# Optimization experiments

Hardware: AMD Instinct MI355X
Metric: run time of the kernel (lower is better)

The kernel has to match this reference:

```python
import jax, jax.numpy as jnp
import numpy as np

B, N, D = 8, 1024, 512
H, DH = 8, 64
CH, CD = 6, 64  # ck/cv come in as (b, 6, n, 64); 6*64 = opn_inner_dim = 384
ID = H * DH    # inner_dim = 512
SCALE = DH ** -0.5


def _l2norm_dim1(x):
    # F.normalize(x, dim=1): normalize over the token axis of (b, n, c)
    return x / jnp.maximum(jnp.linalg.norm(x, axis=1, keepdims=True), 1e-12)


def _style_vectorizer(c, ws, bs):
    b, h, n, d = c.shape
    x = c.transpose(0, 2, 1, 3).reshape(b, n, h * d)
    x = _l2norm_dim1(x)
    for w, bi in zip(ws, bs):
        x = jax.nn.leaky_relu(x @ w.T + bi, 0.2)
    return x.reshape(b, n, H, DH).transpose(0, 2, 1, 3)


def _mlp_block(x, w, b):
    # x: (b, H, n, DH) -> rearr, normalize over n, Linear+GELU(exact), rearr back
    bb, h, n, d = x.shape
    y = x.transpose(0, 2, 1, 3).reshape(bb, n, h * d)
    y = _l2norm_dim1(y)
    y = jax.nn.gelu(y @ w.T + b, approximate=False)
    return y.reshape(bb, n, H, DH).transpose(0, 2, 1, 3)


def setup_inputs() -> dict:
    key = jax.random.key(0)
    ks = jax.random.split(key, 24)
    s = 0.02  # keep attention logits well-conditioned
    return {
        "x": jax.random.normal(ks[0], (B, N, D), jnp.float32),
        "ck": jax.random.normal(ks[1], (B, CH, N, CD), jnp.float32),
        "cv": jax.random.normal(ks[2], (B, CH, N, CD), jnp.float32),
        "w_qkv": jax.random.normal(ks[3], (3 * ID, D), jnp.float32) * s,
        "w_out": jax.random.normal(ks[4], (D, ID), jnp.float32) * s,
        "b_out": jnp.zeros((D,), jnp.float32),
        "ckw0": jax.random.normal(ks[5], (ID, CH * CD), jnp.float32) * s,
        "ckb0": jnp.zeros((ID,), jnp.float32),
        "ckw1": jax.random.normal(ks[6], (ID, ID), jnp.float32) * s,
        "ckb1": jnp.zeros((ID,), jnp.float32),
        "ckw2": jax.random.normal(ks[7], (ID, ID), jnp.float32) * s,
        "ckb2": jnp.zeros((ID,), jnp.float32),
        "cvw0": jax.random.normal(ks[8], (ID, CH * CD), jnp.float32) * s,
        "cvb0": jnp.zeros((ID,), jnp.float32),
        "cvw1": jax.random.normal(ks[9], (ID, ID), jnp.float32) * s,
        "cvb1": jnp.zeros((ID,), jnp.float32),
        "cvw2": jax.random.normal(ks[10], (ID, ID), jnp.float32) * s,
        "cvb2": jnp.zeros((ID,), jnp.float32),
        "nl_w": jax.random.normal(ks[11], (ID, ID), jnp.float32) * s,
        "nl_b": jnp.zeros((ID,), jnp.float32),
        "sub_ratio": jax.random.normal(ks[12], (1, H, 1, DH), jnp.float32) + 1.0,
    }


def reference(x, ck, cv, w_qkv, w_out, b_out,
              ckw0, ckb0, ckw1, ckb1, ckw2, ckb2,
              cvw0, cvb0, cvw1, cvb1, cvw2, cvb2,
              nl_w, nl_b, sub_ratio):
    b, n, _ = x.shape
    qkv = x @ w_qkv.T                      # (b, n, 3*ID)
    q, k, v = jnp.split(qkv, 3, axis=-1)
    to_h = lambda t: t.reshape(b, n, H, DH).transpose(0, 2, 1, 3)  # (b,H,n,DH)
    q, k, v = to_h(q), to_h(k), to_h(v)

    # standard self-attention branch
    dots = jnp.einsum("bhnd,bhmd->bhnm", q, k) * SCALE
    out = jnp.einsum("bhnm,bhmd->bhnd", jax.nn.softmax(dots, axis=-1), v)

    # context (correction) branch
    ckh = _style_vectorizer(ck, (ckw0, ckw1, ckw2), (ckb0, ckb1, ckb2))
    cvh = _style_vectorizer(cv, (cvw0, cvw1, cvw2), (cvb0, cvb1, cvb2))
    dots_c = jnp.einsum("bhnd,bhmd->bhnm", q, ckh) * SCALE
    out_c = jnp.einsum("bhnm,bhmd->bhnd", jax.nn.softmax(dots_c, axis=-1), cvh)
    out_c = _mlp_block(out_c, nl_w, nl_b)

    out = out - out_c * sub_ratio          # elementwise scale-subtract combine
    out = out.transpose(0, 2, 1, 3).reshape(b, n, ID)
    return out @ w_out.T + b_out
```

## Files before the change

kernel.cpp:

```cpp
#include <hip/hip_runtime.h>
#include <hip/hip_fp16.h>
#include <math.h>

typedef _Float16 h16_t;
typedef __attribute__((ext_vector_type(4))) _Float16 h16x4;
typedef __attribute__((ext_vector_type(8))) _Float16 h16x8;
typedef __attribute__((ext_vector_type(4))) float f32x4;

static_assert(sizeof(h16_t) == 2, "f16 size");

__device__ __forceinline__ f32x4 mfma16(h16x8 a, h16x8 b, f32x4 c) {
  return __builtin_amdgcn_mfma_f32_16x16x32_f16(a, b, c, 0, 0, 0);
}

struct CvtArgs {
  const float* src[10];
  h16_t* dst[10];
  int start4[10];
  int total4;
};

__global__ __launch_bounds__(256) void k_cvt_multi(CvtArgs a) {
  const int i4 = blockIdx.x * 256 + threadIdx.x;
  if (i4 >= a.total4) return;
  int seg = 0;
#pragma unroll
  for (int t = 1; t < 10; ++t) seg += (i4 >= a.start4[t]) ? 1 : 0;
  const int off = (i4 - a.start4[seg]) * 4;
  const float4 v = *(const float4*)(a.src[seg] + off);
  h16x4 o;
  o[0] = (h16_t)v.x; o[1] = (h16_t)v.y; o[2] = (h16_t)v.z; o[3] = (h16_t)v.w;
  *(h16x4*)(a.dst[seg] + off) = o;
}

template <int K>
__device__ __forceinline__ void gemm_run(const h16_t* __restrict__ A,
                                         const h16_t* __restrict__ W,
                                         int m0, int o0, h16_t* wl, f32x4* acc) {
  constexpr int NS = K / 128;
  const int lane = threadIdx.x & 63;
  const int l15 = lane & 15;
  const int quad = lane >> 4;
  int sr[4], sc[4], sd[4];
#pragma unroll
  for (int i = 0; i < 4; ++i) {
    const int id = threadIdx.x + i * 256;
    const int row = id >> 4, c = id & 15;
    sr[i] = row;
    sc[i] = c * 8;
    sd[i] = (row * 16 + (c ^ (row & 7))) * 8;
  }
  h16x8 wr[4];
#pragma unroll
  for (int i = 0; i < 4; ++i)
    wr[i] = *(const h16x8*)(W + (size_t)(o0 + sr[i]) * K + sc[i]);
#pragma unroll
  for (int i = 0; i < 4; ++i) *(h16x8*)(wl + sd[i]) = wr[i];
  __syncthreads();
#pragma unroll
  for (int sg = 0; sg < NS; ++sg) {
    if (sg + 1 < NS) {
#pragma unroll
      for (int i = 0; i < 4; ++i)
        wr[i] = *(const h16x8*)(W + (size_t)(o0 + sr[i]) * K + (sg + 1) * 128 + sc[i]);
    }
    const h16_t* ap = A + (size_t)(m0 + l15) * K + sg * 128 + quad * 8;
    const h16_t* wp = wl + (sg & 1) * 8192;
#pragma unroll
    for (int ks = 0; ks < 4; ++ks) {
      h16x8 af = *(const h16x8*)(ap + ks * 32);
#pragma unroll
      for (int j = 0; j < 4; ++j) {
        h16x8 wf = *(const h16x8*)(
            wp + (size_t)((j * 16 + l15) * 16 + ((ks * 4 + quad) ^ (l15 & 7))) * 8);
        acc[j] = mfma16(af, wf, acc[j]);
      }
    }
    if (sg + 1 < NS) {
      h16_t* wn = wl + ((sg + 1) & 1) * 8192;
#pragma unroll
      for (int i = 0; i < 4; ++i) *(h16x8*)(wn + sd[i]) = wr[i];
    }
    __syncthreads();
  }
}

#define EPILOGUE_SETUP()                            \
  const int wv = threadIdx.x >> 6;                  \
  const int lane = threadIdx.x & 63;                \
  const int l15 = lane & 15;                        \
  const int quad = lane >> 4;                       \
  const int m0 = blockIdx.x * 64 + wv * 16;         \
  const int o0 = blockIdx.y * 64;                   \
  f32x4 acc[4];                                     \
  for (int j = 0; j < 4; ++j) acc[j] = f32x4{0.f, 0.f, 0.f, 0.f};

__global__ __launch_bounds__(256) void k_gemm_qkv(
    const h16_t* __restrict__ X, const h16_t* __restrict__ W,
    h16_t* __restrict__ qb, h16_t* __restrict__ kb, h16_t* __restrict__ vT) {
  __shared__ h16_t wl[2 * 8192];
  EPILOGUE_SETUP();
  gemm_run<512>(X, W, m0, o0, wl, acc);
#pragma unroll
  for (int j = 0; j < 4; ++j)
#pragma unroll
    for (int r = 0; r < 4; ++r) {
      const int o = o0 + j * 16 + l15;
      const int m = m0 + quad * 4 + r;
      const int b = m >> 10, n = m & 1023;
      const int oo = o & 511, h = oo >> 6, d = oo & 63;
      const size_t bh = (size_t)(b * 8 + h);
      const h16_t v = (h16_t)acc[j][r];
      if (o < 512)
        qb[(bh * 1024 + n) * 64 + d] = v;
      else if (o < 1024)
        kb[(bh * 1024 + n) * 64 + d] = v;
      else
        vT[(bh * 64 + d) * 1024 + n] = v;
    }
}

struct Leaky2Args {
  const h16_t* A0; const h16_t* W0; const float* b0; h16_t* Y0;
  const h16_t* A1; const h16_t* W1; const float* b1; h16_t* Y1;
};

template <int K, int L0, int L1>
__global__ __launch_bounds__(256) void k_gemm_leaky2(Leaky2Args g) {
  __shared__ h16_t wl[2 * 8192];
  const int zz = blockIdx.z;
  const h16_t* A = zz ? g.A1 : g.A0;
  const h16_t* W = zz ? g.W1 : g.W0;
  const float* bias = zz ? g.b1 : g.b0;
  h16_t* Y = zz ? g.Y1 : g.Y0;
  EPILOGUE_SETUP();
  gemm_run<K>(A, W, m0, o0, wl, acc);
  const int LAYOUT = zz ? L1 : L0;
#pragma unroll
  for (int j = 0; j < 4; ++j)
#pragma unroll
    for (int r = 0; r < 4; ++r) {
      const int o = o0 + j * 16 + l15;
      const int m = m0 + quad * 4 + r;
      float v = acc[j][r] + bias[o];
      v = v > 0.f ? v : 0.2f * v;
      if (LAYOUT == 0) {
        Y[(size_t)m * 512 + o] = (h16_t)v;
      } else {
        const int b = m >> 10, n = m & 1023;
        const int h = o >> 6, d = o & 63;
        if (LAYOUT == 1)
          Y[((size_t)(b * 8 + h) * 1024 + n) * 64 + d] = (h16_t)v;
        else
          Y[((size_t)(b * 8 + h) * 64 + d) * 1024 + n] = (h16_t)v;
      }
    }
}

__global__ __launch_bounds__(256) void k_gemm_nl(
    const h16_t* __restrict__ A, const h16_t* __restrict__ W,
    const float* __restrict__ bias, const h16_t* __restrict__ attn,
    const float* __restrict__ subr, h16_t* __restrict__ Y) {
  __shared__ h16_t wl[2 * 8192];
  EPILOGUE_SETUP();
  gemm_run<512>(A, W, m0, o0, wl, acc);
#pragma unroll
  for (int j = 0; j < 4; ++j)
#pragma unroll
    for (int r = 0; r < 4; ++r) {
      const int o = o0 + j * 16 + l15;
      const int m = m0 + quad * 4 + r;
      const float v = acc[j][r] + bias[o];
      const float g = 0.5f * v * (1.f + erff(v * 0.70710678118654752f));
      const float res = (float)attn[(size_t)m * 512 + o] - g * subr[o];
      Y[(size_t)m * 512 + o] = (h16_t)res;
    }
}

__global__ __launch_bounds__(256) void k_gemm_out(
    const h16_t* __restrict__ A, const h16_t* __restrict__ W,
    const float* __restrict__ bias, float* __restrict__ Y) {
  __shared__ h16_t wl[2 * 8192];
  EPILOGUE_SETUP();
  gemm_run<512>(A, W, m0, o0, wl, acc);
#pragma unroll
  for (int j = 0; j < 4; ++j)
#pragma unroll
    for (int r = 0; r < 4; ++r) {
      const int o = o0 + j * 16 + l15;
      const int m = m0 + quad * 4 + r;
      Y[(size_t)m * 512 + o] = acc[j][r] + bias[o];
    }
}

__global__ __launch_bounds__(256) void k_attn4(
    const h16_t* __restrict__ q,
    const h16_t* __restrict__ k0, const h16_t* __restrict__ v0, h16_t* __restrict__ out0,
    const h16_t* __restrict__ k1, const h16_t* __restrict__ v1, h16_t* __restrict__ out1) {
  const int wv = threadIdx.x >> 6;
  const int lane = threadIdx.x & 63;
  const int l15 = lane & 15;
  const int quad = lane >> 4;
  const int bh = blockIdx.y, b = bh >> 3, h = bh & 7;
  const h16_t* kb = (blockIdx.z ? k1 : k0) + (size_t)bh * 65536;
  const h16_t* vb = (blockIdx.z ? v1 : v0) + (size_t)bh * 65536;
  h16_t* out = blockIdx.z ? out1 : out0;

  __shared__ h16_t kls[2 * 4096];
  __shared__ h16_t vls[2 * 4096];

  const int q0r = blockIdx.x * 128 + wv * 32;
  h16x8 qa[2][2];
#pragma unroll
  for (int t = 0; t < 2; ++t)
#pragma unroll
    for (int s = 0; s < 2; ++s)
      qa[t][s] = *(const h16x8*)(q + ((size_t)bh * 1024 + q0r + t * 16 + l15) * 64 + s * 32 + quad * 8);

  int ksrc[2], vsrc[2], ldst[2];
#pragma unroll
  for (int i = 0; i < 2; ++i) {
    const int L = threadIdx.x + i * 256;
    const int row = L >> 3, cs = L & 7;
    const int key = ((row & 3) << 1) | ((row >> 3) & 1);
    const int c = cs ^ key;
    ksrc[i] = row * 64 + c * 8;
    vsrc[i] = row * 1024 + c * 8;
    ldst[i] = L * 8;
  }

  int kfo[2][4], vfo[2][4];
#pragma unroll
  for (int s = 0; s < 2; ++s)
#pragma unroll
    for (int nt = 0; nt < 4; ++nt) {
      const int r = (nt & 1) * 32 + (l15 >> 2) * 8 + (nt >> 1) * 4 + (l15 & 3);
      const int kk = ((r & 3) << 1) | ((r >> 3) & 1);
      kfo[s][nt] = (r * 8 + ((s * 4 + quad) ^ kk)) * 8;
      const int d = nt * 16 + l15;
      const int kd = ((d & 3) << 1) | ((d >> 3) & 1);
      vfo[s][nt] = (d * 8 + ((s * 4 + quad) ^ kd)) * 8;
    }

  f32x4 oaT[2][4];
#pragma unroll
  for (int t = 0; t < 2; ++t)
#pragma unroll
    for (int j = 0; j < 4; ++j) oaT[t][j] = f32x4{0.f, 0.f, 0.f, 0.f};
  float l_part[2] = {0.f, 0.f};

  h16x8 kr[2], vr[2];
#pragma unroll
  for (int i = 0; i < 2; ++i) {
    kr[i] = *(const h16x8*)(kb + ksrc[i]);
    vr[i] = *(const h16x8*)(vb + vsrc[i]);
  }
#pragma unroll
  for (int i = 0; i < 2; ++i) {
    *(h16x8*)(kls + ldst[i]) = kr[i];
    *(h16x8*)(vls + ldst[i]) = vr[i];
  }
  __syncthreads();

  for (int mt = 0; mt < 16; ++mt) {
    const int cur = (mt & 1) * 4096;
    if (mt < 15) {
      const int mm1 = (mt + 1) * 64;
#pragma unroll
      for (int i = 0; i < 2; ++i) {
        kr[i] = *(const h16x8*)(kb + mm1 * 64 + ksrc[i]);
        vr[i] = *(const h16x8*)(vb + mm1 + vsrc[i]);
      }
    }

    f32x4 sfT[2][4];
#pragma unroll
    for (int t = 0; t < 2; ++t)
#pragma unroll
      for (int j = 0; j < 4; ++j) sfT[t][j] = f32x4{0.f, 0.f, 0.f, 0.f};
#pragma unroll
    for (int s = 0; s < 2; ++s)
#pragma unroll
      for (int nt = 0; nt < 4; ++nt) {
        h16x8 kf = *(const h16x8*)(kls + cur + kfo[s][nt]);
        sfT[0][nt] = mfma16(kf, qa[0][s], sfT[0][nt]);
        sfT[1][nt] = mfma16(kf, qa[1][s], sfT[1][nt]);
      }
    int pk[2][4][2];
#pragma unroll
    for (int t = 0; t < 2; ++t)
#pragma unroll
      for (int nt = 0; nt < 4; ++nt) {
        const float e0 = __expf(sfT[t][nt][0] * 0.125f);
        const float e1 = __expf(sfT[t][nt][1] * 0.125f);
        const float e2 = __expf(sfT[t][nt][2] * 0.125f);
        const float e3 = __expf(sfT[t][nt][3] * 0.125f);
        l_part[t] += (e0 + e1) + (e2 + e3);
        pk[t][nt][0] = __builtin_bit_cast(int, __builtin_amdgcn_cvt_pkrtz(e0, e1));
        pk[t][nt][1] = __builtin_bit_cast(int, __builtin_amdgcn_cvt_pkrtz(e2, e3));
      }
#pragma unroll
    for (int s = 0; s < 2; ++s) {
      int4 b0 = {pk[0][s][0], pk[0][s][1], pk[0][s + 2][0], pk[0][s + 2][1]};
      int4 b1 = {pk[1][s][0], pk[1][s][1], pk[1][s + 2][0], pk[1][s + 2][1]};
      h16x8 bf0 = __builtin_bit_cast(h16x8, b0);
      h16x8 bf1 = __builtin_bit_cast(h16x8, b1);
#pragma unroll
      for (int nt = 0; nt < 4; ++nt) {
        h16x8 vf = *(const h16x8*)(vls + cur + vfo[s][nt]);
        oaT[0][nt] = mfma16(vf, bf0, oaT[0][nt]);
        oaT[1][nt] = mfma16(vf, bf1, oaT[1][nt]);
      }
    }

    if (mt < 15) {
      const int nxt = ((mt + 1) & 1) * 4096;
#pragma unroll
      for (int i = 0; i < 2; ++i) {
        *(h16x8*)(kls + nxt + ldst[i]) = kr[i];
        *(h16x8*)(vls + nxt + ldst[i]) = vr[i];
      }
    }
    __syncthreads();
  }
#pragma unroll
  for (int t = 0; t < 2; ++t) {
    float l = l_part[t] + __shfl_xor(l_part[t], 16, 64);
    l += __shfl_xor(l, 32, 64);
    const float iv = 1.f / l;
    h16_t* obase = out + ((size_t)b * 1024 + q0r + t * 16 + l15) * 512 + h * 64 + quad * 4;
#pragma unroll
    for (int nt = 0; nt < 4; ++nt) {
      h16x4 o;
#pragma unroll
      for (int r = 0; r < 4; ++r) o[r] = (h16_t)(oaT[t][nt][r] * iv);
      *(h16x4*)(obase + nt * 16) = o;
    }
  }
}

__global__ __launch_bounds__(384) void k_cn_ck_p1(const float* __restrict__ c0,
                                                  const float* __restrict__ c1,
                                                  float* __restrict__ part) {
  const int b = blockIdx.x, ch = blockIdx.y, z = blockIdx.z, f = threadIdx.x;
  const float* c = z ? c1 : c0;
  const int h = f >> 6, d = f & 63;
  const float* p = c + ((size_t)(b * 6 + h) * 1024 + ch * 16) * 64 + d;
  float s = 0.f;
#pragma unroll
  for (int n = 0; n < 16; ++n) {
    const float v = p[(size_t)n * 64];
    s += v * v;
  }
  part[(size_t)z * 196608 + (size_t)(b * 64 + ch) * 384 + f] = s;
}

__global__ __launch_bounds__(384) void k_cn_ck_p2(const float* __restrict__ part,
                                                  float* __restrict__ inv) {
  const int b = blockIdx.x, z = blockIdx.y, f = threadIdx.x;
  float s = 0.f;
#pragma unroll 8
  for (int ch = 0; ch < 64; ++ch)
    s += part[(size_t)z * 196608 + (size_t)(b * 64 + ch) * 384 + f];
  inv[z * 3072 + b * 384 + f] = 1.f / fmaxf(sqrtf(s), 1e-12f);
}

__global__ __launch_bounds__(384) void k_norm_ck(const float* __restrict__ c0,
                                                 const float* __restrict__ c1,
                                                 const float* __restrict__ inv,
                                                 h16_t* __restrict__ y0,
                                                 h16_t* __restrict__ y1) {
  const int bn = blockIdx.x, z = blockIdx.y, f = threadIdx.x;
  const float* c = z ? c1 : c0;
  h16_t* out = z ? y1 : y0;
  const int b = bn >> 10, n = bn & 1023;
  const int h = f >> 6, d = f & 63;
  out[(size_t)bn * 384 + f] =
      (h16_t)(c[((size_t)(b * 6 + h) * 1024 + n) * 64 + d] * inv[z * 3072 + b * 384 + f]);
}

__global__ __launch_bounds__(512) void k_cn_rm_p1(const h16_t* __restrict__ a,
                                                  float* __restrict__ part) {
  const int b = blockIdx.x, ch = blockIdx.y, f = threadIdx.x;
  const h16_t* p = a + ((size_t)b * 1024 + ch * 16) * 512 + f;
  float s = 0.f;
#pragma unroll
  for (int n = 0; n < 16; ++n) {
    const float v = (float)p[(size_t)n * 512];
    s += v * v;
  }
  part[(size_t)(b * 64 + ch) * 512 + f] = s;
}

__global__ __launch_bounds__(512) void k_cn_rm_p2(const float* __restrict__ part,
                                                  float* __restrict__ inv) {
  const int b = blockIdx.x, f = threadIdx.x;
  float s = 0.f;
#pragma unroll 8
  for (int ch = 0; ch < 64; ++ch) s += part[(size_t)(b * 64 + ch) * 512 + f];
  inv[b * 512 + f] = 1.f / fmaxf(sqrtf(s), 1e-12f);
}

__global__ __launch_bounds__(512) void k_norm_rm(const h16_t* __restrict__ a,
                                                 const float* __restrict__ inv,
                                                 h16_t* __restrict__ out) {
  const int bn = blockIdx.x, f = threadIdx.x;
  const int b = bn >> 10;
  out[(size_t)bn * 512 + f] = (h16_t)((float)a[(size_t)bn * 512 + f] * inv[b * 512 + f]);
}

extern "C" void kernel_launch(void* const* d_in, const int* in_sizes, int n_in,
                              void* d_out, int out_size, void* d_ws, size_t ws_size,
                              hipStream_t stream) {
  (void)in_sizes; (void)n_in; (void)out_size; (void)ws_size;
  const float* x     = (const float*)d_in[0];
  const float* ck    = (const float*)d_in[1];
  const float* cv    = (const float*)d_in[2];
  const float* w_qkv = (const float*)d_in[3];
  const float* w_out = (const float*)d_in[4];
  const float* b_out = (const float*)d_in[5];
  const float* ckw0  = (const float*)d_in[6];
  const float* ckb0  = (const float*)d_in[7];
  const float* ckw1  = (const float*)d_in[8];
  const float* ckb1  = (const float*)d_in[9];
  const float* ckw2  = (const float*)d_in[10];
  const float* ckb2  = (const float*)d_in[11];
  const float* cvw0  = (const float*)d_in[12];
  const float* cvb0  = (const float*)d_in[13];
  const float* cvw1  = (const float*)d_in[14];
  const float* cvb1  = (const float*)d_in[15];
  const float* cvw2  = (const float*)d_in[16];
  const float* cvb2  = (const float*)d_in[17];
  const float* nl_w  = (const float*)d_in[18];
  const float* nl_b  = (const float*)d_in[19];
  const float* subr  = (const float*)d_in[20];

  const size_t MB = 1024 * 1024;
  char* p = (char*)d_ws;
  float* inv1 = (float*)p;
  float* part = (float*)(p + 64 * 1024);
  h16_t* S0 = (h16_t*)(p + 2 * MB + 0 * 8 * MB);
  h16_t* S1 = (h16_t*)(p + 2 * MB + 1 * 8 * MB);
  h16_t* S2 = (h16_t*)(p + 2 * MB + 2 * 8 * MB);
  h16_t* S3 = (h16_t*)(p + 2 * MB + 3 * 8 * MB);
  h16_t* S4 = (h16_t*)(p + 2 * MB + 4 * 8 * MB);
  h16_t* S5 = (h16_t*)(p + 2 * MB + 5 * 8 * MB);
  h16_t* WBASE = (h16_t*)(p + 50 * MB);
  h16_t* w_qkvb = WBASE;
  h16_t* w_outb = w_qkvb + 786432;
  h16_t* ckw0b  = w_outb + 262144;
  h16_t* ckw1b  = ckw0b + 196608;
  h16_t* ckw2b  = ckw1b + 262144;
  h16_t* cvw0b  = ckw2b + 262144;
  h16_t* cvw1b  = cvw0b + 196608;
  h16_t* cvw2b  = cvw1b + 262144;
  h16_t* nl_wb  = cvw2b + 262144;
  h16_t* T0   = (h16_t*)d_out;
  h16_t* T1   = (h16_t*)d_out + 4194304;
  h16_t* XB   = S5;
  h16_t* ATTN = T1;

  const dim3 blk(256);
  {
    CvtArgs a;
    const float* srcs[10] = {x, w_qkv, w_out, ckw0, ckw1, ckw2, cvw0, cvw1, cvw2, nl_w};
    h16_t* dsts[10] = {XB, w_qkvb, w_outb, ckw0b, ckw1b, ckw2b, cvw0b, cvw1b, cvw2b, nl_wb};
    const int ns[10] = {4194304, 786432, 262144, 196608, 262144, 262144, 196608, 262144, 262144, 262144};
    int cum = 0;
    for (int i = 0; i < 10; ++i) {
      a.src[i] = srcs[i]; a.dst[i] = dsts[i]; a.start4[i] = cum; cum += ns[i] / 4;
    }
    a.total4 = cum;
    k_cvt_multi<<<(cum + 255) / 256, blk, 0, stream>>>(a);
  }

  k_cn_ck_p1<<<dim3(8, 64, 2), 384, 0, stream>>>(ck, cv, part);
  k_cn_ck_p2<<<dim3(8, 2), 384, 0, stream>>>(part, inv1);
  k_norm_ck<<<dim3(8192, 2), 384, 0, stream>>>(ck, cv, inv1, T0, S0);

  {
    Leaky2Args g = {T0, ckw0b, ckb0, T1, S0, cvw0b, cvb0, S1};
    k_gemm_leaky2<384, 0, 0><<<dim3(128, 8, 2), blk, 0, stream>>>(g);
  }
  {
    Leaky2Args g = {T1, ckw1b, ckb1, T0, S1, cvw1b, cvb1, S0};
    k_gemm_leaky2<512, 0, 0><<<dim3(128, 8, 2), blk, 0, stream>>>(g);
  }
  {
    Leaky2Args g = {T0, ckw2b, ckb2, S3, S0, cvw2b, cvb2, S4};
    k_gemm_leaky2<512, 1, 2><<<dim3(128, 8, 2), blk, 0, stream>>>(g);
  }

  k_gemm_qkv<<<dim3(128, 24), blk, 0, stream>>>(XB, w_qkvb, S0, S1, S2);

  k_attn4<<<dim3(8, 64, 2), blk, 0, stream>>>(S0, S1, S2, ATTN, S3, S4, S5);

  k_cn_rm_p1<<<dim3(8, 64), 512, 0, stream>>>(S5, part);
  k_cn_rm_p2<<<8, 512, 0, stream>>>(part, inv1);
  k_norm_rm<<<8192, 512, 0, stream>>>(S5, inv1, T0);
  k_gemm_nl<<<dim3(128, 8), blk, 0, stream>>>(T0, nl_wb, nl_b, ATTN, subr, S1);
  k_gemm_out<<<dim3(128, 8), blk, 0, stream>>>(S1, w_outb, b_out, (float*)d_out);
}
```

Baseline: 352.9 us.

## Merge QKV projection GEMM into first style-vectorizer GEMM launch

Folds the QKV projection GEMM and the first leaky-ReLU layer of both style vectorizers into one launch of 5120 blocks, split by block index. Buffers are reassigned so the q/k/v outputs survive the later vectorizer layers, which needs new scratch placements for ATTN and the normalized input. This removes one kernel launch and its tail, and lets the two independent GEMMs fill the GPU together. The cost is one kernel holding both code paths, which may raise register pressure, and a more tangled buffer aliasing plan.

New measurement: 351.5 us. No clear change (-0.4%).

```diff
diff --git a/kernel.cpp b/kernel.cpp
--- a/kernel.cpp
+++ b/kernel.cpp
@@ -94,31 +94,6 @@
   const int o0 = blockIdx.y * 64;                   \
   f32x4 acc[4];                                     \
   for (int j = 0; j < 4; ++j) acc[j] = f32x4{0.f, 0.f, 0.f, 0.f};
-
-__global__ __launch_bounds__(256) void k_gemm_qkv(
-    const h16_t* __restrict__ X, const h16_t* __restrict__ W,
-    h16_t* __restrict__ qb, h16_t* __restrict__ kb, h16_t* __restrict__ vT) {
-  __shared__ h16_t wl[2 * 8192];
-  EPILOGUE_SETUP();
-  gemm_run<512>(X, W, m0, o0, wl, acc);
-#pragma unroll
-  for (int j = 0; j < 4; ++j)
-#pragma unroll
-    for (int r = 0; r < 4; ++r) {
-      const int o = o0 + j * 16 + l15;
-      const int m = m0 + quad * 4 + r;
-      const int b = m >> 10, n = m & 1023;
-      const int oo = o & 511, h = oo >> 6, d = oo & 63;
-      const size_t bh = (size_t)(b * 8 + h);
-      const h16_t v = (h16_t)acc[j][r];
-      if (o < 512)
-        qb[(bh * 1024 + n) * 64 + d] = v;
-      else if (o < 1024)
-        kb[(bh * 1024 + n) * 64 + d] = v;
-      else
-        vT[(bh * 64 + d) * 1024 + n] = v;
-    }
-}
 
 struct Leaky2Args {
   const h16_t* A0; const h16_t* W0; const float* b0; h16_t* Y0;
@@ -155,6 +130,63 @@
           Y[((size_t)(b * 8 + h) * 64 + d) * 1024 + n] = (h16_t)v;
       }
     }
+}
+
+__global__ __launch_bounds__(256) void k_g0_qkv(
+    Leaky2Args g, const h16_t* __restrict__ X, const h16_t* __restrict__ Wq,
+    h16_t* __restrict__ qb, h16_t* __restrict__ kb, h16_t* __restrict__ vT) {
+  __shared__ h16_t wl[2 * 8192];
+  const int bid = blockIdx.x;
+  const int wv = threadIdx.x >> 6;
+  const int lane = threadIdx.x & 63;
+  const int l15 = lane & 15;
+  const int quad = lane >> 4;
+  f32x4 acc[4];
+#pragma unroll
+  for (int j = 0; j < 4; ++j) acc[j] = f32x4{0.f, 0.f, 0.f, 0.f};
+
+  if (bid < 2048) {
+    const int zz = bid >> 10;
+    const int m0 = (bid & 127) * 64 + wv * 16;
+    const int o0 = ((bid >> 7) & 7) * 64;
+    const h16_t* A = zz ? g.A1 : g.A0;
+    const h16_t* W = zz ? g.W1 : g.W0;
+    const float* bias = zz ? g.b1 : g.b0;
+    h16_t* Y = zz ? g.Y1 : g.Y0;
+    gemm_run<384>(A, W, m0, o0, wl, acc);
+#pragma unroll
+    for (int j = 0; j < 4; ++j)
+#pragma unroll
+      for (int r = 0; r < 4; ++r) {
+        const int o = o0 + j * 16 + l15;
+        const int m = m0 + quad * 4 + r;
+        float v = acc[j][r] + bias[o];
+        v = v > 0.f ? v : 0.2f * v;
+        Y[(size_t)m * 512 + o] = (h16_t)v;
+      }
+  } else {
+    const int q = bid - 2048;
+    const int m0 = (q & 127) * 64 + wv * 16;
+    const int o0 = (q >> 7) * 64;
+    gemm_run<512>(X, Wq, m0, o0, wl, acc);
+#pragma unroll
+    for (int j = 0; j < 4; ++j)
+#pragma unroll
+      for (int r = 0; r < 4; ++r) {
+        const int o = o0 + j * 16 + l15;
+        const int m = m0 + quad * 4 + r;
+        const int b = m >> 10, n = m & 1023;
+        const int oo = o & 511, h = oo >> 6, d = oo & 63;
+        const size_t bh = (size_t)(b * 8 + h);
+        const h16_t v = (h16_t)acc[j][r];
+        if (o < 512)
+          qb[(bh * 1024 + n) * 64 + d] = v;
+        else if (o < 1024)
+          kb[(bh * 1024 + n) * 64 + d] = v;
+        else
+          vT[(bh * 64 + d) * 1024 + n] = v;
+      }
+  }
 }
 
 __global__ __launch_bounds__(256) void k_gemm_nl(
@@ -458,7 +490,7 @@
   h16_t* T0   = (h16_t*)d_out;
   h16_t* T1   = (h16_t*)d_out + 4194304;
   h16_t* XB   = S5;
-  h16_t* ATTN = T1;
+  h16_t* ATTN = T0;
 
   const dim3 blk(256);
   {
@@ -480,24 +512,23 @@
 
   {
     Leaky2Args g = {T0, ckw0b, ckb0, T1, S0, cvw0b, cvb0, S1};
-    k_gemm_leaky2<384, 0, 0><<<dim3(128, 8, 2), blk, 0, stream>>>(g);
-  }
+    k_g0_qkv<<<5120, blk, 0, stream>>>(g, XB, w_qkvb, S2, S3, S4);
+  }
+
   {
     Leaky2Args g = {T1, ckw1b, ckb1, T0, S1, cvw1b, cvb1, S0};
     k_gemm_leaky2<512, 0, 0><<<dim3(128, 8, 2), blk, 0, stream>>>(g);
   }
   {
-    Leaky2Args g = {T0, ckw2b, ckb2, S3, S0, cvw2b, cvb2, S4};
+    Leaky2Args g = {T0, ckw2b, ckb2, T1, S0, cvw2b, cvb2, S1};
     k_gemm_leaky2<512, 1, 2><<<dim3(128, 8, 2), blk, 0, stream>>>(g);
   }
 
-  k_gemm_qkv<<<dim3(128, 24), blk, 0, stream>>>(XB, w_qkvb, S0, S1, S2);
-
-  k_attn4<<<dim3(8, 64, 2), blk, 0, stream>>>(S0, S1, S2, ATTN, S3, S4, S5);
+  k_attn4<<<dim3(8, 64, 2), blk, 0, stream>>>(S2, S3, S4, ATTN, T1, S1, S5);
 
   k_cn_rm_p1<<<dim3(8, 64), 512, 0, stream>>>(S5, part);
   k_cn_rm_p2<<<8, 512, 0, stream>>>(part, inv1);
-  k_norm_rm<<<8192, 512, 0, stream>>>(S5, inv1, T0);
-  k_gemm_nl<<<dim3(128, 8), blk, 0, stream>>>(T0, nl_wb, nl_b, ATTN, subr, S1);
+  k_norm_rm<<<8192, 512, 0, stream>>>(S5, inv1, S0);
+  k_gemm_nl<<<dim3(128, 8), blk, 0, stream>>>(S0, nl_wb, nl_b, ATTN, subr, S1);
   k_gemm_out<<<dim3(128, 8), blk, 0, stream>>>(S1, w_outb, b_out, (float*)d_out);
 }
```
